# Optimization experiments

Hardware: AMD Instinct MI355X
Metric: run time of the kernel (lower is better)

## Reference

```python
import jax, jax.numpy as jnp
import numpy as np
import math

B, L, H, E = 16, 1024, 8, 64   # L = nsensor = N (forced by einsum 'bhls,bhlg')
WIN = 1024                      # win_size, last dim of x
G = 64                          # n_group
D_SEL = 1                       # d_sel default


def setup_inputs() -> dict:
    key = jax.random.key(0)
    ks = jax.random.split(key, 7)
    return {
        "queries": jax.random.normal(ks[0], (B, L, H, E), dtype=jnp.float32),
        "keys": jax.random.normal(ks[1], (B, L, H, E), dtype=jnp.float32),
        "values": jax.random.normal(ks[2], (B, L, H, E), dtype=jnp.float32),
        "x": jax.random.normal(ks[3], (B, L, WIN), dtype=jnp.float32),
        "mlp_w": jax.random.normal(ks[4], (H * D_SEL, WIN), dtype=jnp.float32) * 0.02,
        "mlp_b": jax.random.normal(ks[5], (H * D_SEL,), dtype=jnp.float32) * 0.02,
        "sel_W": jax.random.normal(ks[6], (H, G, D_SEL), dtype=jnp.float32),
        "attn_mask": 0,
    }


def _select_attention(x, mlp_w, mlp_b, sel_W, n_heads, d_sel):
    b, n, lwin = x.shape
    xf = x.reshape(b * n, lwin)
    newx = jnp.tanh(xf @ mlp_w.T + mlp_b)                 # [(B*N), H*d_sel]
    # Faithful raw reshape (torch.reshape, no permute): mixes n and h axes.
    newx = newx.reshape(b, n_heads, n, d_sel)             # [B, H, N, d_sel]
    sel = jnp.einsum('bhnd,hgd->bhng', newx, sel_W)       # [B, H, N, G]
    return jax.nn.relu(sel)


def reference(queries, keys, values, x, mlp_w, mlp_b, sel_W, attn_mask):
    b, l, h, e = queries.shape
    scale = 1.0 / math.sqrt(e)
    scores = jnp.einsum('blhe,bshe->bhls', queries, keys)      # [B, H, L, S]
    sel = _select_attention(x, mlp_w, mlp_b, sel_W, h, D_SEL)  # [B, H, L, G]
    scores = jnp.einsum('bhls,bhlg->bhsg', scores, sel)        # [B, H, S, G]
    series = jax.nn.softmax(scale * scores, axis=-1)           # softmax over groups
    # values labeled 'blhs': l=S (value len), s=D (feature). Output V: [B, D, H, G]
    V = jnp.einsum('blhs,bhlg->bshg', values, series)
    return V
```

## Files before the change

### kernel.cpp

```cpp
#include <hip/hip_runtime.h>
#include <math.h>

#define NB 16
#define NL 1024
#define NH 8
#define NE 64
#define NWIN 1024
#define NG 64

#define SCH 128
#define SROW 136

typedef __attribute__((ext_vector_type(8))) short short8;
typedef __attribute__((ext_vector_type(4))) float floatx4;

__device__ __forceinline__ short f2bf(float x) {
    unsigned u = __float_as_uint(x);
    u += 0x7fffu + ((u >> 16) & 1u);
    return (short)(u >> 16);
}
__device__ __forceinline__ float dot4(float4 a, float4 b) {
    return fmaf(a.x, b.x, fmaf(a.y, b.y, fmaf(a.z, b.z, a.w * b.w)));
}

__global__ __launch_bounds__(256) void k_sel_q(
    const float* __restrict__ x, const float* __restrict__ mlp_w,
    const float* __restrict__ mlp_b, const float* __restrict__ q,
    float* __restrict__ qp, float* __restrict__ qn)
{
    __shared__ float4 w_lds[8][NWIN / 4];
    __shared__ float t_lds[128];
    __shared__ float redp[4][64], redn[4][64];

    int tid = threadIdx.x;
    int blk = blockIdx.x;
    int qq = blk & 7, bh = blk >> 3;
    int b = bh >> 3, h = bh & 7;
    int w = tid >> 6, lane = tid & 63;

    const float4* w4 = (const float4*)mlp_w;
    float4* wl = (float4*)w_lds;
    #pragma unroll
    for (int i = 0; i < 8; ++i)
        wl[tid + 256 * i] = w4[tid + 256 * i];
    __syncthreads();

    int r0 = b * 1024 + h * 128 + qq * 16 + w * 4;
    float bc = mlp_b[lane & 7];
    float4 xa[4], xb[4];
    {
        const float4* p0 = (const float4*)(x + (size_t)r0 * NWIN);
        #pragma unroll
        for (int it = 0; it < 4; ++it) xa[it] = p0[it * 64 + lane];
    }
    #pragma unroll
    for (int j = 0; j < 4; ++j) {
        if (j < 3) {
            const float4* pn = (const float4*)(x + (size_t)(r0 + j + 1) * NWIN);
            #pragma unroll
            for (int it = 0; it < 4; ++it) xb[it] = pn[it * 64 + lane];
        }
        float o0=0,o1=0,o2=0,o3=0,o4=0,o5=0,o6=0,o7=0;
        #pragma unroll
        for (int it = 0; it < 4; ++it) {
            float4 xv = xa[it];
            o0 += dot4(xv, w_lds[0][it * 64 + lane]);
            o1 += dot4(xv, w_lds[1][it * 64 + lane]);
            o2 += dot4(xv, w_lds[2][it * 64 + lane]);
            o3 += dot4(xv, w_lds[3][it * 64 + lane]);
            o4 += dot4(xv, w_lds[4][it * 64 + lane]);
            o5 += dot4(xv, w_lds[5][it * 64 + lane]);
            o6 += dot4(xv, w_lds[6][it * 64 + lane]);
            o7 += dot4(xv, w_lds[7][it * 64 + lane]);
        }
        o0 += __shfl_xor(o0, 1, 64); o1 += __shfl_xor(o1, 1, 64);
        o2 += __shfl_xor(o2, 1, 64); o3 += __shfl_xor(o3, 1, 64);
        o4 += __shfl_xor(o4, 1, 64); o5 += __shfl_xor(o5, 1, 64);
        o6 += __shfl_xor(o6, 1, 64); o7 += __shfl_xor(o7, 1, 64);
        bool b0 = lane & 1;
        float m0 = b0 ? o1 : o0, m1 = b0 ? o3 : o2;
        float m2 = b0 ? o5 : o4, m3 = b0 ? o7 : o6;
        m0 += __shfl_xor(m0, 2, 64); m1 += __shfl_xor(m1, 2, 64);
        m2 += __shfl_xor(m2, 2, 64); m3 += __shfl_xor(m3, 2, 64);
        bool b1 = lane & 2;
        float n0 = b1 ? m1 : m0, n1 = b1 ? m3 : m2;
        n0 += __shfl_xor(n0, 4, 64); n1 += __shfl_xor(n1, 4, 64);
        float q0 = (lane & 4) ? n1 : n0;
        q0 += __shfl_xor(q0, 8, 64);
        q0 += __shfl_xor(q0, 16, 64);
        q0 += __shfl_xor(q0, 32, 64);
        if (lane < 8)
            t_lds[w * 32 + j * 8 + lane] = tanhf(q0 + bc);
        #pragma unroll
        for (int it = 0; it < 4; ++it) xa[it] = xb[it];
    }

    int lo = lane >> 4, e4 = lane & 15;
    float4 accp = make_float4(0,0,0,0), accn = make_float4(0,0,0,0);
    #pragma unroll
    for (int i = 0; i < 8; ++i) {
        int l_loc = w * 32 + i * 4 + lo;
        float tv = t_lds[l_loc];
        int l = qq * 128 + l_loc;
        float4 qv = *(const float4*)(q + (((size_t)(b * NL + l)) * NH + h) * NE + e4 * 4);
        float tp = fmaxf(tv, 0.f), tn = fminf(tv, 0.f);
        accp.x = fmaf(tp, qv.x, accp.x); accp.y = fmaf(tp, qv.y, accp.y);
        accp.z = fmaf(tp, qv.z, accp.z); accp.w = fmaf(tp, qv.w, accp.w);
        accn.x = fmaf(tn, qv.x, accn.x); accn.y = fmaf(tn, qv.y, accn.y);
        accn.z = fmaf(tn, qv.z, accn.z); accn.w = fmaf(tn, qv.w, accn.w);
    }
    #pragma unroll
    for (int off = 16; off <= 32; off <<= 1) {
        accp.x += __shfl_xor(accp.x, off, 64); accp.y += __shfl_xor(accp.y, off, 64);
        accp.z += __shfl_xor(accp.z, off, 64); accp.w += __shfl_xor(accp.w, off, 64);
        accn.x += __shfl_xor(accn.x, off, 64); accn.y += __shfl_xor(accn.y, off, 64);
        accn.z += __shfl_xor(accn.z, off, 64); accn.w += __shfl_xor(accn.w, off, 64);
    }
    if (lo == 0) {
        *(float4*)&redp[w][e4 * 4] = accp;
        *(float4*)&redn[w][e4 * 4] = accn;
    }
    __syncthreads();
    if (tid < 64) {
        atomicAdd(&qp[bh * NE + tid], redp[0][tid] + redp[1][tid] + redp[2][tid] + redp[3][tid]);
    } else if (tid < 128) {
        int e = tid - 64;
        atomicAdd(&qn[bh * NE + e], redn[0][e] + redn[1][e] + redn[2][e] + redn[3][e]);
    }
}

__global__ __launch_bounds__(256, 4) void k_attn_out(
    const float* __restrict__ keys, const float* __restrict__ values,
    const float* __restrict__ sel_W,
    const float* __restrict__ qp, const float* __restrict__ qn,
    float* __restrict__ partial)
{
    __shared__ short sb[NG][SROW];
    __shared__ float ap_l[SCH], an_l[SCH];
    __shared__ float2 wpn[NG];
    __shared__ float mx2[2][SCH], dn2[2][SCH];

    int tid = threadIdx.x, blk = blockIdx.x;
    int chunk = blk & 7, bh = blk >> 3;
    int b = bh >> 3, h = bh & 7;
    int w = tid >> 6, lane = tid & 63;
    int c = lane & 15, sq = lane >> 4;
    const float scale = 0.125f;
    int s0 = chunk * SCH;

    float vreg[32];
    const float* vbase = values + (((size_t)(b * NL + s0)) * NH + h) * NE + 16 * w + c;
    #pragma unroll
    for (int ks = 0; ks < 4; ++ks)
        #pragma unroll
        for (int j = 0; j < 8; ++j)
            vreg[ks * 8 + j] = vbase[(size_t)(ks * 32 + sq * 8 + j) * (NH * NE)];

    if (tid < NG) {
        float W = sel_W[h * NG + tid];
        wpn[tid] = make_float2(fmaxf(W, 0.f) * scale, fminf(W, 0.f) * scale);
    }
    const float4 qp4 = *(const float4*)(qp + bh * NE + c * 4);
    const float4 qn4 = *(const float4*)(qn + bh * NE + c * 4);

    #pragma unroll
    for (int p = 0; p < 8; ++p) {
        int sl = w * 32 + p * 4 + sq;
        float4 kv = *(const float4*)(keys + (((size_t)(b * NL + s0 + sl)) * NH + h) * NE + c * 4);
        float pp = dot4(kv, qp4);
        float pn = dot4(kv, qn4);
        #pragma unroll
        for (int m_ = 1; m_ <= 8; m_ <<= 1) {
            pp += __shfl_xor(pp, m_, 64);
            pn += __shfl_xor(pn, m_, 64);
        }
        if (c == 0) { ap_l[sl] = pp; an_l[sl] = pn; }
    }
    __syncthreads();

    {
        int s_ = tid & 127, gh = tid >> 7, g0 = gh * 32;
        float ap = ap_l[s_], an = an_l[s_];
        float m = -1e30f;
        #pragma unroll 8
        for (int g = 0; g < 32; ++g) {
            float2 wv = wpn[g0 + g];
            m = fmaxf(m, fmaf(wv.x, ap, wv.y * an));
        }
        mx2[gh][s_] = m;
        __syncthreads();
        m = fmaxf(mx2[0][s_], mx2[1][s_]);
        float d = 0.f;
        #pragma unroll 8
        for (int g = 0; g < 32; ++g) {
            float2 wv = wpn[g0 + g];
            d += __expf(fmaf(wv.x, ap, wv.y * an) - m);
        }
        dn2[gh][s_] = d;
        __syncthreads();
        float inv = 1.0f / (dn2[0][s_] + dn2[1][s_]);
        #pragma unroll 8
        for (int g = 0; g < 32; ++g) {
            float2 wv = wpn[g0 + g];
            sb[g0 + g][s_] = f2bf(__expf(fmaf(wv.x, ap, wv.y * an) - m) * inv);
        }
    }
    __syncthreads();

    floatx4 acc[4] = {{0.f,0.f,0.f,0.f},{0.f,0.f,0.f,0.f},
                      {0.f,0.f,0.f,0.f},{0.f,0.f,0.f,0.f}};
    #pragma unroll
    for (int ks = 0; ks < 4; ++ks) {
        short8 av;
        #pragma unroll
        for (int j = 0; j < 8; ++j) av[j] = f2bf(vreg[ks * 8 + j]);
        #pragma unroll
        for (int n = 0; n < 4; ++n) {
            short8 bv = *(const short8*)&sb[16 * n + c][ks * 32 + sq * 8];
            acc[n] = __builtin_amdgcn_mfma_f32_16x16x32_bf16(av, bv, acc[n], 0, 0, 0);
        }
    }

    float* pch = partial + (size_t)chunk * (NB * NE * NH * NG);
    #pragma unroll
    for (int n = 0; n < 4; ++n) {
        #pragma unroll
        for (int r = 0; r < 4; ++r) {
            int e = 16 * w + sq * 4 + r;
            int g = 16 * n + c;
            pch[((size_t)(b * NE + e) * NH + h) * NG + g] = acc[n][r];
        }
    }
}

__global__ __launch_bounds__(256) void k_reduce(
    const float* __restrict__ partial, float* __restrict__ out)
{
    int i = blockIdx.x * 256 + threadIdx.x;
    const float4* p = (const float4*)partial;
    float4 s = p[i];
    #pragma unroll
    for (int ch = 1; ch < 8; ++ch) {
        float4 t = p[(size_t)ch * 131072 + i];
        s.x += t.x; s.y += t.y; s.z += t.z; s.w += t.w;
    }
    ((float4*)out)[i] = s;
}

extern "C" void kernel_launch(void* const* d_in, const int* in_sizes, int n_in,
                              void* d_out, int out_size, void* d_ws, size_t ws_size,
                              hipStream_t stream) {
    (void)in_sizes; (void)n_in; (void)ws_size; (void)out_size;
    const float* queries = (const float*)d_in[0];
    const float* keys    = (const float*)d_in[1];
    const float* values  = (const float*)d_in[2];
    const float* x       = (const float*)d_in[3];
    const float* mlp_w   = (const float*)d_in[4];
    const float* mlp_b   = (const float*)d_in[5];
    const float* sel_W   = (const float*)d_in[6];
    float* out = (float*)d_out;

    float* partial = (float*)d_ws;
    float* qp_ws = partial + 8 * (NB * NE * NH * NG);
    float* qn_ws = qp_ws + NB * NH * NE;

    hipMemsetAsync(qp_ws, 0, (size_t)2 * NB * NH * NE * sizeof(float), stream);

    k_sel_q<<<dim3(NB * NH * 8), dim3(256), 0, stream>>>(x, mlp_w, mlp_b,
                                                          queries, qp_ws, qn_ws);
    k_attn_out<<<dim3(NB * NH * 8), dim3(256), 0, stream>>>(keys, values, sel_W,
                                                            qp_ws, qn_ws, partial);
    k_reduce<<<dim3(512), dim3(256), 0, stream>>>(partial, out);
}
```

Measured before the change: 202.7 us.

## Split attention chunks finer and restructure MLP to keep weights in registers

The attention-output kernel now uses 16 chunks of 64 sequence positions instead of 8 chunks of 128. This doubles the grid and the occupancy hint, and the values are converted to bf16 fragments at load time. The selection MLP kernel drops the LDS copy of mlp_w: each wave holds a quarter of the window dimension in registers, processes all 16 rows per block, and reduces across waves through shared memory. The cost is twice the partial-sum buffer, which raises global write and read traffic in the reduce kernel.

```diff
diff --git a/kernel.cpp b/kernel.cpp
--- a/kernel.cpp
+++ b/kernel.cpp
@@ -8,8 +8,9 @@
 #define NWIN 1024
 #define NG 64
 
-#define SCH 128
-#define SROW 136
+#define SCH 64
+#define SROW 72
+#define NCH 16
 
 typedef __attribute__((ext_vector_type(8))) short short8;
 typedef __attribute__((ext_vector_type(4))) float floatx4;
@@ -23,77 +24,71 @@
     return fmaf(a.x, b.x, fmaf(a.y, b.y, fmaf(a.z, b.z, a.w * b.w)));
 }
 
-__global__ __launch_bounds__(256) void k_sel_q(
+__global__ __launch_bounds__(256, 5) void k_sel_q(
     const float* __restrict__ x, const float* __restrict__ mlp_w,
     const float* __restrict__ mlp_b, const float* __restrict__ q,
     float* __restrict__ qp, float* __restrict__ qn)
 {
-    __shared__ float4 w_lds[8][NWIN / 4];
+    __shared__ float red[4][16][64];
     __shared__ float t_lds[128];
     __shared__ float redp[4][64], redn[4][64];
 
-    int tid = threadIdx.x;
-    int blk = blockIdx.x;
-    int qq = blk & 7, bh = blk >> 3;
+    int tid = threadIdx.x, blk = blockIdx.x;
+    int oct = blk & 7, bh = blk >> 3;
     int b = bh >> 3, h = bh & 7;
     int w = tid >> 6, lane = tid & 63;
 
-    const float4* w4 = (const float4*)mlp_w;
-    float4* wl = (float4*)w_lds;
-    #pragma unroll
-    for (int i = 0; i < 8; ++i)
-        wl[tid + 256 * i] = w4[tid + 256 * i];
-    __syncthreads();
-
-    int r0 = b * 1024 + h * 128 + qq * 16 + w * 4;
-    float bc = mlp_b[lane & 7];
-    float4 xa[4], xb[4];
-    {
-        const float4* p0 = (const float4*)(x + (size_t)r0 * NWIN);
-        #pragma unroll
-        for (int it = 0; it < 4; ++it) xa[it] = p0[it * 64 + lane];
-    }
-    #pragma unroll
-    for (int j = 0; j < 4; ++j) {
-        if (j < 3) {
-            const float4* pn = (const float4*)(x + (size_t)(r0 + j + 1) * NWIN);
-            #pragma unroll
-            for (int it = 0; it < 4; ++it) xb[it] = pn[it * 64 + lane];
-        }
-        float o0=0,o1=0,o2=0,o3=0,o4=0,o5=0,o6=0,o7=0;
-        #pragma unroll
-        for (int it = 0; it < 4; ++it) {
-            float4 xv = xa[it];
-            o0 += dot4(xv, w_lds[0][it * 64 + lane]);
-            o1 += dot4(xv, w_lds[1][it * 64 + lane]);
-            o2 += dot4(xv, w_lds[2][it * 64 + lane]);
-            o3 += dot4(xv, w_lds[3][it * 64 + lane]);
-            o4 += dot4(xv, w_lds[4][it * 64 + lane]);
-            o5 += dot4(xv, w_lds[5][it * 64 + lane]);
-            o6 += dot4(xv, w_lds[6][it * 64 + lane]);
-            o7 += dot4(xv, w_lds[7][it * 64 + lane]);
-        }
-        o0 += __shfl_xor(o0, 1, 64); o1 += __shfl_xor(o1, 1, 64);
-        o2 += __shfl_xor(o2, 1, 64); o3 += __shfl_xor(o3, 1, 64);
-        o4 += __shfl_xor(o4, 1, 64); o5 += __shfl_xor(o5, 1, 64);
-        o6 += __shfl_xor(o6, 1, 64); o7 += __shfl_xor(o7, 1, 64);
-        bool b0 = lane & 1;
-        float m0 = b0 ? o1 : o0, m1 = b0 ? o3 : o2;
-        float m2 = b0 ? o5 : o4, m3 = b0 ? o7 : o6;
-        m0 += __shfl_xor(m0, 2, 64); m1 += __shfl_xor(m1, 2, 64);
-        m2 += __shfl_xor(m2, 2, 64); m3 += __shfl_xor(m3, 2, 64);
-        bool b1 = lane & 2;
-        float n0 = b1 ? m1 : m0, n1 = b1 ? m3 : m2;
-        n0 += __shfl_xor(n0, 4, 64); n1 += __shfl_xor(n1, 4, 64);
-        float q0 = (lane & 4) ? n1 : n0;
-        q0 += __shfl_xor(q0, 8, 64);
-        q0 += __shfl_xor(q0, 16, 64);
-        q0 += __shfl_xor(q0, 32, 64);
-        if (lane < 8)
-            t_lds[w * 32 + j * 8 + lane] = tanhf(q0 + bc);
-        #pragma unroll
-        for (int it = 0; it < 4; ++it) xa[it] = xb[it];
-    }
+    float4 w4[8];
+    const float* wq = mlp_w + w * 256 + lane * 4;
+    #pragma unroll
+    for (int c = 0; c < 8; ++c)
+        w4[c] = *(const float4*)(wq + (size_t)c * NWIN);
+
+    int r0 = b * 1024 + h * 128 + oct * 16;
+    const float* xbase = x + (size_t)r0 * NWIN + w * 256 + lane * 4;
+
+    #pragma unroll
+    for (int batch = 0; batch < 2; ++batch) {
+        float4 xv[8];
+        #pragma unroll
+        for (int j = 0; j < 8; ++j)
+            xv[j] = *(const float4*)(xbase + (size_t)(batch * 8 + j) * NWIN);
+        #pragma unroll
+        for (int j = 0; j < 8; ++j) {
+            float o0 = dot4(xv[j], w4[0]), o1 = dot4(xv[j], w4[1]);
+            float o2 = dot4(xv[j], w4[2]), o3 = dot4(xv[j], w4[3]);
+            float o4 = dot4(xv[j], w4[4]), o5 = dot4(xv[j], w4[5]);
+            float o6 = dot4(xv[j], w4[6]), o7 = dot4(xv[j], w4[7]);
+            o0 += __shfl_xor(o0, 1, 64); o1 += __shfl_xor(o1, 1, 64);
+            o2 += __shfl_xor(o2, 1, 64); o3 += __shfl_xor(o3, 1, 64);
+            o4 += __shfl_xor(o4, 1, 64); o5 += __shfl_xor(o5, 1, 64);
+            o6 += __shfl_xor(o6, 1, 64); o7 += __shfl_xor(o7, 1, 64);
+            bool b0 = lane & 1;
+            float m0 = b0 ? o1 : o0, m1 = b0 ? o3 : o2;
+            float m2 = b0 ? o5 : o4, m3 = b0 ? o7 : o6;
+            m0 += __shfl_xor(m0, 2, 64); m1 += __shfl_xor(m1, 2, 64);
+            m2 += __shfl_xor(m2, 2, 64); m3 += __shfl_xor(m3, 2, 64);
+            bool b1 = lane & 2;
+            float n0 = b1 ? m1 : m0, n1 = b1 ? m3 : m2;
+            n0 += __shfl_xor(n0, 4, 64); n1 += __shfl_xor(n1, 4, 64);
+            float f = (lane & 4) ? n1 : n0;
+            red[w][batch * 8 + j][(lane & 7) * 8 + (lane >> 3)] = f;
+        }
+    }
+    __syncthreads();
+
+    if (tid < 128) {
+        int j = tid >> 3, c = tid & 7;
+        float s = 0.f;
+        #pragma unroll
+        for (int w2 = 0; w2 < 4; ++w2) {
+            float4 a = *(const float4*)&red[w2][j][c * 8];
+            float4 d = *(const float4*)&red[w2][j][c * 8 + 4];
+            s += a.x + a.y + a.z + a.w + d.x + d.y + d.z + d.w;
+        }
+        t_lds[tid] = tanhf(s + mlp_b[c]);
+    }
+    __syncthreads();
 
     int lo = lane >> 4, e4 = lane & 15;
     float4 accp = make_float4(0,0,0,0), accn = make_float4(0,0,0,0);
@@ -101,7 +96,7 @@
     for (int i = 0; i < 8; ++i) {
         int l_loc = w * 32 + i * 4 + lo;
         float tv = t_lds[l_loc];
-        int l = qq * 128 + l_loc;
+        int l = oct * 128 + l_loc;
         float4 qv = *(const float4*)(q + (((size_t)(b * NL + l)) * NH + h) * NE + e4 * 4);
         float tp = fmaxf(tv, 0.f), tn = fminf(tv, 0.f);
         accp.x = fmaf(tp, qv.x, accp.x); accp.y = fmaf(tp, qv.y, accp.y);
@@ -129,7 +124,7 @@
     }
 }
 
-__global__ __launch_bounds__(256, 4) void k_attn_out(
+__global__ __launch_bounds__(256, 8) void k_attn_out(
     const float* __restrict__ keys, const float* __restrict__ values,
     const float* __restrict__ sel_W,
     const float* __restrict__ qp, const float* __restrict__ qn,
@@ -138,23 +133,28 @@
     __shared__ short sb[NG][SROW];
     __shared__ float ap_l[SCH], an_l[SCH];
     __shared__ float2 wpn[NG];
-    __shared__ float mx2[2][SCH], dn2[2][SCH];
+    __shared__ float mx4[4][SCH], dn4[4][SCH];
 
     int tid = threadIdx.x, blk = blockIdx.x;
-    int chunk = blk & 7, bh = blk >> 3;
+    int chunk = blk & (NCH - 1), bh = blk >> 4;
     int b = bh >> 3, h = bh & 7;
     int w = tid >> 6, lane = tid & 63;
     int c = lane & 15, sq = lane >> 4;
     const float scale = 0.125f;
     int s0 = chunk * SCH;
 
-    float vreg[32];
+    short8 av[2];
     const float* vbase = values + (((size_t)(b * NL + s0)) * NH + h) * NE + 16 * w + c;
     #pragma unroll
-    for (int ks = 0; ks < 4; ++ks)
+    for (int ks = 0; ks < 2; ++ks) {
+        float tmp[8];
         #pragma unroll
         for (int j = 0; j < 8; ++j)
-            vreg[ks * 8 + j] = vbase[(size_t)(ks * 32 + sq * 8 + j) * (NH * NE)];
+            tmp[j] = vbase[(size_t)(ks * 32 + sq * 8 + j) * (NH * NE)];
+        #pragma unroll
+        for (int j = 0; j < 8; ++j) av[ks][j] = f2bf(tmp[j]);
+    }
+    __builtin_amdgcn_sched_barrier(0);
 
     if (tid < NG) {
         float W = sel_W[h * NG + tid];
@@ -164,8 +164,8 @@
     const float4 qn4 = *(const float4*)(qn + bh * NE + c * 4);
 
     #pragma unroll
-    for (int p = 0; p < 8; ++p) {
-        int sl = w * 32 + p * 4 + sq;
+    for (int p = 0; p < 4; ++p) {
+        int sl = w * 16 + p * 4 + sq;
         float4 kv = *(const float4*)(keys + (((size_t)(b * NL + s0 + sl)) * NH + h) * NE + c * 4);
         float pp = dot4(kv, qp4);
         float pn = dot4(kv, qn4);
@@ -179,28 +179,28 @@
     __syncthreads();
 
     {
-        int s_ = tid & 127, gh = tid >> 7, g0 = gh * 32;
+        int s_ = tid & 63, q4 = tid >> 6, g0 = q4 * 16;
         float ap = ap_l[s_], an = an_l[s_];
         float m = -1e30f;
-        #pragma unroll 8
-        for (int g = 0; g < 32; ++g) {
+        #pragma unroll
+        for (int g = 0; g < 16; ++g) {
             float2 wv = wpn[g0 + g];
             m = fmaxf(m, fmaf(wv.x, ap, wv.y * an));
         }
-        mx2[gh][s_] = m;
+        mx4[q4][s_] = m;
         __syncthreads();
-        m = fmaxf(mx2[0][s_], mx2[1][s_]);
+        m = fmaxf(fmaxf(mx4[0][s_], mx4[1][s_]), fmaxf(mx4[2][s_], mx4[3][s_]));
         float d = 0.f;
-        #pragma unroll 8
-        for (int g = 0; g < 32; ++g) {
+        #pragma unroll
+        for (int g = 0; g < 16; ++g) {
             float2 wv = wpn[g0 + g];
             d += __expf(fmaf(wv.x, ap, wv.y * an) - m);
         }
-        dn2[gh][s_] = d;
+        dn4[q4][s_] = d;
         __syncthreads();
-        float inv = 1.0f / (dn2[0][s_] + dn2[1][s_]);
-        #pragma unroll 8
-        for (int g = 0; g < 32; ++g) {
+        float inv = 1.0f / (dn4[0][s_] + dn4[1][s_] + dn4[2][s_] + dn4[3][s_]);
+        #pragma unroll
+        for (int g = 0; g < 16; ++g) {
             float2 wv = wpn[g0 + g];
             sb[g0 + g][s_] = f2bf(__expf(fmaf(wv.x, ap, wv.y * an) - m) * inv);
         }
@@ -210,14 +210,11 @@
     floatx4 acc[4] = {{0.f,0.f,0.f,0.f},{0.f,0.f,0.f,0.f},
                       {0.f,0.f,0.f,0.f},{0.f,0.f,0.f,0.f}};
     #pragma unroll
-    for (int ks = 0; ks < 4; ++ks) {
-        short8 av;
-        #pragma unroll
-        for (int j = 0; j < 8; ++j) av[j] = f2bf(vreg[ks * 8 + j]);
+    for (int ks = 0; ks < 2; ++ks) {
         #pragma unroll
         for (int n = 0; n < 4; ++n) {
             short8 bv = *(const short8*)&sb[16 * n + c][ks * 32 + sq * 8];
-            acc[n] = __builtin_amdgcn_mfma_f32_16x16x32_bf16(av, bv, acc[n], 0, 0, 0);
+            acc[n] = __builtin_amdgcn_mfma_f32_16x16x32_bf16(av[ks], bv, acc[n], 0, 0, 0);
         }
     }
 
@@ -240,7 +237,7 @@
     const float4* p = (const float4*)partial;
     float4 s = p[i];
     #pragma unroll
-    for (int ch = 1; ch < 8; ++ch) {
+    for (int ch = 1; ch < NCH; ++ch) {
         float4 t = p[(size_t)ch * 131072 + i];
         s.x += t.x; s.y += t.y; s.z += t.z; s.w += t.w;
     }
@@ -261,14 +258,14 @@
     float* out = (float*)d_out;
 
     float* partial = (float*)d_ws;
-    float* qp_ws = partial + 8 * (NB * NE * NH * NG);
+    float* qp_ws = partial + (size_t)NCH * (NB * NE * NH * NG);
     float* qn_ws = qp_ws + NB * NH * NE;
 
     hipMemsetAsync(qp_ws, 0, (size_t)2 * NB * NH * NE * sizeof(float), stream);
 
     k_sel_q<<<dim3(NB * NH * 8), dim3(256), 0, stream>>>(x, mlp_w, mlp_b,
                                                           queries, qp_ws, qn_ws);
-    k_attn_out<<<dim3(NB * NH * 8), dim3(256), 0, stream>>>(keys, values, sel_W,
-                                                            qp_ws, qn_ws, partial);
+    k_attn_out<<<dim3(NB * NH * NCH), dim3(256), 0, stream>>>(keys, values, sel_W,
+                                                              qp_ws, qn_ws, partial);
     k_reduce<<<dim3(512), dim3(256), 0, stream>>>(partial, out);
 }
```

Result: no change. 201.9 us (-0.4%).

## Split attention into 16 sequence chunks, reorder block index, prefetch keys

Applied to the files above, without the earlier changes.

Halves the sequence chunk per block in the attention-output kernel (128→64) and doubles the number of chunks, so the grid has twice as many blocks. Block indices are reordered so heads vary fastest in both kernels, which changes locality for x/keys/values reads. Key loads are hoisted next to the value loads ahead of a scheduling barrier so more memory traffic is in flight at once. In exchange, the partial-sum buffer doubles in size, which adds write traffic plus a longer reduction, and the minimum-occupancy hint on the launch bounds is dropped.

```diff
diff --git a/kernel.cpp b/kernel.cpp
--- a/kernel.cpp
+++ b/kernel.cpp
@@ -8,8 +8,9 @@
 #define NWIN 1024
 #define NG 64
 
-#define SCH 128
-#define SROW 136
+#define SCH 64
+#define SROW 72
+#define NCH 16
 
 typedef __attribute__((ext_vector_type(8))) short short8;
 typedef __attribute__((ext_vector_type(4))) float floatx4;
@@ -34,8 +35,10 @@
 
     int tid = threadIdx.x;
     int blk = blockIdx.x;
-    int qq = blk & 7, bh = blk >> 3;
-    int b = bh >> 3, h = bh & 7;
+    int h = blk & 7;
+    int qq = (blk >> 3) & 7;
+    int b = blk >> 6;
+    int bh = b * 8 + h;
     int w = tid >> 6, lane = tid & 63;
 
     const float4* w4 = (const float4*)mlp_w;
@@ -129,7 +132,7 @@
     }
 }
 
-__global__ __launch_bounds__(256, 4) void k_attn_out(
+__global__ __launch_bounds__(256) void k_attn_out(
     const float* __restrict__ keys, const float* __restrict__ values,
     const float* __restrict__ sel_W,
     const float* __restrict__ qp, const float* __restrict__ qn,
@@ -138,23 +141,32 @@
     __shared__ short sb[NG][SROW];
     __shared__ float ap_l[SCH], an_l[SCH];
     __shared__ float2 wpn[NG];
-    __shared__ float mx2[2][SCH], dn2[2][SCH];
+    __shared__ float mx4[4][SCH], dn4[4][SCH];
 
     int tid = threadIdx.x, blk = blockIdx.x;
-    int chunk = blk & 7, bh = blk >> 3;
-    int b = bh >> 3, h = bh & 7;
+    int h = blk & 7;
+    int chunk = (blk >> 3) & (NCH - 1);
+    int b = blk >> 7;
+    int bh = b * 8 + h;
     int w = tid >> 6, lane = tid & 63;
     int c = lane & 15, sq = lane >> 4;
     const float scale = 0.125f;
     int s0 = chunk * SCH;
 
-    float vreg[32];
+    float vt[16];
     const float* vbase = values + (((size_t)(b * NL + s0)) * NH + h) * NE + 16 * w + c;
     #pragma unroll
-    for (int ks = 0; ks < 4; ++ks)
+    for (int ks = 0; ks < 2; ++ks)
         #pragma unroll
         for (int j = 0; j < 8; ++j)
-            vreg[ks * 8 + j] = vbase[(size_t)(ks * 32 + sq * 8 + j) * (NH * NE)];
+            vt[ks * 8 + j] = vbase[(size_t)(ks * 32 + sq * 8 + j) * (NH * NE)];
+    float4 k4[4];
+    #pragma unroll
+    for (int p = 0; p < 4; ++p) {
+        int sl = w * 16 + p * 4 + sq;
+        k4[p] = *(const float4*)(keys + (((size_t)(b * NL + s0 + sl)) * NH + h) * NE + c * 4);
+    }
+    __builtin_amdgcn_sched_barrier(0);
 
     if (tid < NG) {
         float W = sel_W[h * NG + tid];
@@ -164,11 +176,10 @@
     const float4 qn4 = *(const float4*)(qn + bh * NE + c * 4);
 
     #pragma unroll
-    for (int p = 0; p < 8; ++p) {
-        int sl = w * 32 + p * 4 + sq;
-        float4 kv = *(const float4*)(keys + (((size_t)(b * NL + s0 + sl)) * NH + h) * NE + c * 4);
-        float pp = dot4(kv, qp4);
-        float pn = dot4(kv, qn4);
+    for (int p = 0; p < 4; ++p) {
+        int sl = w * 16 + p * 4 + sq;
+        float pp = dot4(k4[p], qp4);
+        float pn = dot4(k4[p], qn4);
         #pragma unroll
         for (int m_ = 1; m_ <= 8; m_ <<= 1) {
             pp += __shfl_xor(pp, m_, 64);
@@ -179,28 +190,28 @@
     __syncthreads();
 
     {
-        int s_ = tid & 127, gh = tid >> 7, g0 = gh * 32;
+        int s_ = tid & 63, q4i = tid >> 6, g0 = q4i * 16;
         float ap = ap_l[s_], an = an_l[s_];
         float m = -1e30f;
-        #pragma unroll 8
-        for (int g = 0; g < 32; ++g) {
+        #pragma unroll
+        for (int g = 0; g < 16; ++g) {
             float2 wv = wpn[g0 + g];
             m = fmaxf(m, fmaf(wv.x, ap, wv.y * an));
         }
-        mx2[gh][s_] = m;
+        mx4[q4i][s_] = m;
         __syncthreads();
-        m = fmaxf(mx2[0][s_], mx2[1][s_]);
+        m = fmaxf(fmaxf(mx4[0][s_], mx4[1][s_]), fmaxf(mx4[2][s_], mx4[3][s_]));
         float d = 0.f;
-        #pragma unroll 8
-        for (int g = 0; g < 32; ++g) {
+        #pragma unroll
+        for (int g = 0; g < 16; ++g) {
             float2 wv = wpn[g0 + g];
             d += __expf(fmaf(wv.x, ap, wv.y * an) - m);
         }
-        dn2[gh][s_] = d;
+        dn4[q4i][s_] = d;
         __syncthreads();
-        float inv = 1.0f / (dn2[0][s_] + dn2[1][s_]);
-        #pragma unroll 8
-        for (int g = 0; g < 32; ++g) {
+        float inv = 1.0f / (dn4[0][s_] + dn4[1][s_] + dn4[2][s_] + dn4[3][s_]);
+        #pragma unroll
+        for (int g = 0; g < 16; ++g) {
             float2 wv = wpn[g0 + g];
             sb[g0 + g][s_] = f2bf(__expf(fmaf(wv.x, ap, wv.y * an) - m) * inv);
         }
@@ -210,10 +221,10 @@
     floatx4 acc[4] = {{0.f,0.f,0.f,0.f},{0.f,0.f,0.f,0.f},
                       {0.f,0.f,0.f,0.f},{0.f,0.f,0.f,0.f}};
     #pragma unroll
-    for (int ks = 0; ks < 4; ++ks) {
+    for (int ks = 0; ks < 2; ++ks) {
         short8 av;
         #pragma unroll
-        for (int j = 0; j < 8; ++j) av[j] = f2bf(vreg[ks * 8 + j]);
+        for (int j = 0; j < 8; ++j) av[j] = f2bf(vt[ks * 8 + j]);
         #pragma unroll
         for (int n = 0; n < 4; ++n) {
             short8 bv = *(const short8*)&sb[16 * n + c][ks * 32 + sq * 8];
@@ -240,7 +251,7 @@
     const float4* p = (const float4*)partial;
     float4 s = p[i];
     #pragma unroll
-    for (int ch = 1; ch < 8; ++ch) {
+    for (int ch = 1; ch < NCH; ++ch) {
         float4 t = p[(size_t)ch * 131072 + i];
         s.x += t.x; s.y += t.y; s.z += t.z; s.w += t.w;
     }
@@ -261,14 +272,14 @@
     float* out = (float*)d_out;
 
     float* partial = (float*)d_ws;
-    float* qp_ws = partial + 8 * (NB * NE * NH * NG);
+    float* qp_ws = partial + (size_t)NCH * (NB * NE * NH * NG);
     float* qn_ws = qp_ws + NB * NH * NE;
 
     hipMemsetAsync(qp_ws, 0, (size_t)2 * NB * NH * NE * sizeof(float), stream);
 
     k_sel_q<<<dim3(NB * NH * 8), dim3(256), 0, stream>>>(x, mlp_w, mlp_b,
                                                           queries, qp_ws, qn_ws);
-    k_attn_out<<<dim3(NB * NH * 8), dim3(256), 0, stream>>>(keys, values, sel_W,
-                                                            qp_ws, qn_ws, partial);
+    k_attn_out<<<dim3(NB * NH * NCH), dim3(256), 0, stream>>>(keys, values, sel_W,
+                                                              qp_ws, qn_ws, partial);
     k_reduce<<<dim3(512), dim3(256), 0, stream>>>(partial, out);
 }
```

Measured after the change: 201.3 us. About the same (-0.7%).
